# Optimization experiments

Hardware: AMD Instinct MI355X
Metric: run time of the kernel (lower is better)

## Reference

```python
import jax, jax.numpy as jnp
import numpy as np

CH = 256
IC = 128  # inter_channels = channels // reduction
TEMP = 0.05


def setup_inputs() -> dict:
    key = jax.random.key(0)
    k1, k2, k3, k4, k5 = jax.random.split(key, 5)
    x = jax.random.normal(k1, (8, CH, 64, 64), dtype=jnp.float32)
    # 1x1 conv weights stored as [out_ch, in_ch]
    w_qkv = jax.random.normal(k2, (3 * IC, CH), dtype=jnp.float32) * 0.01
    b_qkv = jax.random.normal(k3, (3 * IC,), dtype=jnp.float32) * 0.01
    w_out = jax.random.normal(k4, (CH, IC), dtype=jnp.float32) * 0.01
    b_out = jax.random.normal(k5, (CH,), dtype=jnp.float32) * 0.01
    return {"x": x, "w_qkv": w_qkv, "b_qkv": b_qkv, "w_out": w_out, "b_out": b_out}


def reference(x, w_qkv, b_qkv, w_out, b_out):
    b, c, h, w = x.shape
    n = h * w
    ic = w_qkv.shape[0] // 3
    # 1x1 conv QKV projection
    qkv = jnp.einsum('bchw,oc->bohw', x, w_qkv) + b_qkv[None, :, None, None]
    qkv = qkv.reshape(b, 3, ic, n)
    q, k, v = qkv[:, 0], qkv[:, 1], qkv[:, 2]  # each [b, ic, n]
    # mean-center q and k over spatial positions (per channel)
    k = k - k.mean(axis=-1, keepdims=True)
    q = q - q.mean(axis=-1, keepdims=True)
    # pairwise_weight[b, i, j] = sum_c k[b, c, i] * q[b, c, j]
    pw = jnp.einsum('bci,bcj->bij', k, q)
    pw = pw / jnp.sqrt(jnp.float32(ic))  # use_scale=True
    pw = pw / TEMP
    pw = jax.nn.softmax(pw, axis=-1)  # [b, n, n]
    # y[b, c, i] = sum_j pw[b, i, j] * v[b, c, j]
    y = jnp.einsum('bij,bcj->bci', pw, v).reshape(b, ic, h, w)
    out = x + jnp.einsum('bchw,oc->bohw', y, w_out) + b_out[None, :, None, None]
    return out
```

## Files before the change

### kernel.cpp

```cpp
#include <hip/hip_runtime.h>
#include <hip/hip_bf16.h>

typedef __bf16 bf16_t;
typedef __bf16 bf16x8 __attribute__((ext_vector_type(8)));
typedef float f32x4 __attribute__((ext_vector_type(4)));
typedef float f32x16 __attribute__((ext_vector_type(16)));

#define MFMA16(a, b, c) __builtin_amdgcn_mfma_f32_16x16x32_bf16((a), (b), (c), 0, 0, 0)
#define MFMA32(a, b, c) __builtin_amdgcn_mfma_f32_32x32x16_bf16((a), (b), (c), 0, 0, 0)

constexpr int BATCH = 8, CH = 256, IC = 128, NPOS = 4096;
constexpr float SM_C = 2.5503488f;

constexpr size_t OFF_XT    = 0;
constexpr size_t OFF_QT    = 16777216;
constexpr size_t OFF_KT    = 25165824;
constexpr size_t OFF_V     = 33554432;
constexpr size_t OFF_WQKV  = 41943040;
constexpr size_t OFF_WOUT  = 42139648;
constexpr size_t OFF_XMEAN = 42205184;
constexpr size_t OFF_QKM   = 42213376;
constexpr size_t OFF_PL    = 42221568;

__device__ __forceinline__ void gload_lds16(const char* g, char* lds) {
    __builtin_amdgcn_global_load_lds((const __attribute__((address_space(1))) unsigned int*)g,
                                     (__attribute__((address_space(3))) unsigned int*)lds, 16, 0,
                                     0);
}
__device__ __forceinline__ float fexp2(float x) {
    float r;
    asm("v_exp_f32 %0, %1" : "=v"(r) : "v"(x));
    return r;
}
__device__ __forceinline__ int cvtpk(float lo, float hi) {
    int r;
    asm("v_cvt_pk_bf16_f32 %0, %1, %2" : "=v"(r) : "v"(lo), "v"(hi));
    return r;
}

__global__ void k_convert_w(const float* __restrict__ wqkv, const float* __restrict__ wout,
                            bf16_t* __restrict__ wqkv_b, bf16_t* __restrict__ wout_b) {
    int idx = blockIdx.x * 256 + threadIdx.x;
    if (idx < 384 * 256) wqkv_b[idx] = (bf16_t)wqkv[idx];
    int j = idx - 384 * 256;
    if (j >= 0 && j < 256 * 128) wout_b[j] = (bf16_t)wout[j];
}

__global__ void k_xmean(const float* __restrict__ x, float* __restrict__ xmean) {
    int c = blockIdx.x, b = blockIdx.y;
    const float4* xv = (const float4*)(x + ((size_t)(b * CH + c)) * NPOS);
    float s = 0.f;
#pragma unroll
    for (int r = 0; r < 4; r++) {
        float4 v = xv[r * 256 + threadIdx.x];
        s += v.x + v.y + v.z + v.w;
    }
    __shared__ float red[256];
    red[threadIdx.x] = s;
    __syncthreads();
    for (int st = 128; st > 0; st >>= 1) {
        if (threadIdx.x < st) red[threadIdx.x] += red[threadIdx.x + st];
        __syncthreads();
    }
    if (threadIdx.x == 0) xmean[b * CH + c] = red[0] * (1.0f / NPOS);
}

__global__ void k_qkmean(const float* __restrict__ wqkv, const float* __restrict__ xmean,
                         float* __restrict__ qkm) {
    int o = blockIdx.x, b = blockIdx.y, lane = threadIdx.x;
    float4 w = ((const float4*)(wqkv + (size_t)o * CH))[lane];
    float4 xm = ((const float4*)(xmean + b * CH))[lane];
    float s = w.x * xm.x + w.y * xm.y + w.z * xm.z + w.w * xm.w;
#pragma unroll
    for (int m = 1; m < 64; m <<= 1) s += __shfl_xor(s, m, 64);
    if (lane == 0) qkm[b * CH + o] = s;
}

__global__ void k_transpose(const float* __restrict__ x, bf16_t* __restrict__ xt) {
    __shared__ float t[32][33];
    int p0 = blockIdx.x * 32, c0 = blockIdx.y * 32, b = blockIdx.z;
    int i = threadIdx.x >> 5, j = threadIdx.x & 31;
#pragma unroll
    for (int q = 0; q < 4; q++) {
        int c = c0 + q * 8 + i;
        t[q * 8 + i][j] = x[((size_t)(b * CH + c)) * NPOS + p0 + j];
    }
    __syncthreads();
#pragma unroll
    for (int q = 0; q < 4; q++) {
        int p = p0 + q * 8 + i;
        xt[((size_t)(b * NPOS + p)) * CH + c0 + j] = (bf16_t)t[j][q * 8 + i];
    }
}

__global__ __launch_bounds__(256, 2) void k_qkv(const bf16_t* __restrict__ xt,
                                                const bf16_t* __restrict__ wqkv_b,
                                                const float* __restrict__ qkm,
                                                const float* __restrict__ b_qkv,
                                                bf16_t* __restrict__ qt, bf16_t* __restrict__ kt,
                                                bf16_t* __restrict__ v) {
    int bid = blockIdx.x;
    int b = bid & 7;
    int r0 = bid >> 3;
    int sec = r0 % 3;
    int pt = r0 / 3;
    int p0 = pt * 128;
    int wid = threadIdx.x >> 6, lane = threadIdx.x & 63;
    int g = lane >> 4, li = lane & 15;
    int wr = wid >> 1, wc = wid & 1;
    f32x4 acc[4][4] = {};
    if (sec < 2) {
        int ob = sec * 128;
#pragma unroll 1
        for (int kk = 0; kk < 8; kk++) {
            bf16x8 af[4], bfg[4];
#pragma unroll
            for (int fa = 0; fa < 4; fa++) {
                int p = p0 + wr * 64 + fa * 16 + li;
                af[fa] = *(const bf16x8*)(xt + ((size_t)(b * NPOS + p)) * CH + kk * 32 + g * 8);
            }
#pragma unroll
            for (int fb = 0; fb < 4; fb++) {
                int o = ob + wc * 64 + fb * 16 + li;
                bfg[fb] = *(const bf16x8*)(wqkv_b + (size_t)o * CH + kk * 32 + g * 8);
            }
#pragma unroll
            for (int fa = 0; fa < 4; fa++)
#pragma unroll
                for (int fb = 0; fb < 4; fb++) acc[fa][fb] = MFMA16(af[fa], bfg[fb], acc[fa][fb]);
        }
        bf16_t* dst = (sec == 0) ? qt : kt;
        float scale = (sec == 1) ? SM_C : 1.0f;
#pragma unroll
        for (int fb = 0; fb < 4; fb++) {
            int ol = wc * 64 + fb * 16 + li;
            float mean = qkm[b * CH + sec * 128 + ol];
#pragma unroll
            for (int fa = 0; fa < 4; fa++)
#pragma unroll
                for (int r = 0; r < 4; r++) {
                    int p = p0 + wr * 64 + fa * 16 + g * 4 + r;
                    dst[((size_t)(b * NPOS + p)) * IC + ol] =
                        (bf16_t)((acc[fa][fb][r] - mean) * scale);
                }
        }
    } else {
#pragma unroll 1
        for (int kk = 0; kk < 8; kk++) {
            bf16x8 af[4], bfg[4];
#pragma unroll
            for (int fa = 0; fa < 4; fa++) {
                int o = 256 + wr * 64 + fa * 16 + li;
                af[fa] = *(const bf16x8*)(wqkv_b + (size_t)o * CH + kk * 32 + g * 8);
            }
#pragma unroll
            for (int fb = 0; fb < 4; fb++) {
                int p = p0 + wc * 64 + fb * 16 + li;
                bfg[fb] = *(const bf16x8*)(xt + ((size_t)(b * NPOS + p)) * CH + kk * 32 + g * 8);
            }
#pragma unroll
            for (int fa = 0; fa < 4; fa++)
#pragma unroll
                for (int fb = 0; fb < 4; fb++) acc[fa][fb] = MFMA16(af[fa], bfg[fb], acc[fa][fb]);
        }
#pragma unroll
        for (int fa = 0; fa < 4; fa++)
#pragma unroll
            for (int r = 0; r < 4; r++) {
                int oe = wr * 64 + fa * 16 + g * 4 + r;
                float bias = b_qkv[256 + oe];
#pragma unroll
                for (int fb = 0; fb < 4; fb++) {
                    int p = p0 + wc * 64 + fb * 16 + li;
                    v[((size_t)(b * IC + oe)) * NPOS + p] = (bf16_t)(acc[fa][fb][r] + bias);
                }
            }
    }
}

constexpr int TJ = 64;

__global__ __launch_bounds__(256, 2) void k_attn(const bf16_t* __restrict__ qt,
                                                 const bf16_t* __restrict__ kt,
                                                 const bf16_t* __restrict__ v,
                                                 bf16_t* __restrict__ pacc,
                                                 float* __restrict__ pl) {
    __shared__ __attribute__((aligned(128))) char smem[2 * 32768];
    const int bid = blockIdx.x;
    const int b = bid & 7;
    const int r0 = bid >> 3;
    const int jh = r0 & 1;
    const int it = r0 >> 1;
    const int jbase = jh * 2048;
    const int wid = threadIdx.x >> 6, lane = threadIdx.x & 63;
    const int col = lane & 31, h = lane >> 5;
    const int iw0 = it * 128 + wid * 32;
    const bf16_t* ktb = kt + (size_t)b * NPOS * IC;
    const bf16_t* qtb = qt + (size_t)b * NPOS * IC;
    const bf16_t* vb = v + (size_t)b * IC * NPOS;

    int qoff_[4], voff_[4];
#pragma unroll
    for (int u = 0; u < 4; u++) {
        int t = wid * 4 + u;
        int qrow = 4 * t + (lane >> 4);
        qoff_[u] = qrow * 256 + (((lane & 15) ^ (qrow & 7)) << 4);
        int vrow = 8 * t + (lane >> 3);
        voff_[u] = vrow * 8192 + (((lane & 7) ^ (vrow & 7)) << 4);
    }

    auto stage = [&](int dstpar, int sj) {
        const char* qs = (const char*)qtb + (size_t)sj * 256;
        const char* vs = (const char*)vb + (size_t)sj * 2;
        char* qd = smem + dstpar * 32768;
        char* vd = qd + 16384;
#pragma unroll
        for (int u = 0; u < 4; u++) {
            gload_lds16(qs + qoff_[u], qd + (wid * 4 + u) * 1024);
            gload_lds16(vs + voff_[u], vd + (wid * 4 + u) * 1024);
        }
    };

    stage(0, jbase);

    bf16x8 bk[8];
#pragma unroll
    for (int ks = 0; ks < 8; ks++)
        bk[ks] = *(const bf16x8*)(ktb + (size_t)(iw0 + col) * IC + ks * 16 + h * 8);

    f32x16 acc[4] = {};
    float ls[4] = {0.f, 0.f, 0.f, 0.f};

    auto body = [&](int par, int nextj) {
        stage(par ^ 1, nextj);
        asm volatile("s_waitcnt vmcnt(8)" ::: "memory");
        __builtin_amdgcn_s_barrier();
        asm volatile("" ::: "memory");
        const char* qb = smem + par * 32768;
        const char* vbuf = qb + 16384;
#pragma unroll
        for (int jsub = 0; jsub < 2; jsub++) {
            f32x16 s = {};
#pragma unroll
            for (int ks = 0; ks < 8; ks++) {
                bf16x8 aq = *(const bf16x8*)(qb + (jsub * 32 + col) * 256 +
                                             (((ks * 2 + h) ^ (col & 7)) << 4));
                s = MFMA32(aq, bk[ks], s);
            }
            float e[16];
#pragma unroll
            for (int r = 0; r < 16; r++) e[r] = fexp2(s[r]);
#pragma unroll
            for (int r = 0; r < 16; r++) ls[r & 3] += e[r];
            int w[8];
#pragma unroll
            for (int q = 0; q < 8; q++) w[q] = cvtpk(e[2 * q], e[2 * q + 1]);
            asm("v_permlane32_swap_b32 %0, %1" : "+v"(w[0]), "+v"(w[2]));
            asm("v_permlane32_swap_b32 %0, %1" : "+v"(w[1]), "+v"(w[3]));
            asm("v_permlane32_swap_b32 %0, %1" : "+v"(w[4]), "+v"(w[6]));
            asm("v_permlane32_swap_b32 %0, %1" : "+v"(w[5]), "+v"(w[7]));
            union {
                int u[4];
                bf16x8 v;
            } pb0, pb1;
            pb0.u[0] = w[0]; pb0.u[1] = w[1]; pb0.u[2] = w[2]; pb0.u[3] = w[3];
            pb1.u[0] = w[4]; pb1.u[1] = w[5]; pb1.u[2] = w[6]; pb1.u[3] = w[7];
#pragma unroll
            for (int kl = 0; kl < 2; kl++) {
                int kg = jsub * 2 + kl;
                bf16x8 pbf = kl == 0 ? pb0.v : pb1.v;
#pragma unroll
                for (int cs = 0; cs < 4; cs++) {
                    bf16x8 av = *(const bf16x8*)(vbuf + (cs * 32 + col) * 128 +
                                                 (((kg * 2 + h) ^ (col & 7)) << 4));
                    acc[cs] = MFMA32(av, pbf, acc[cs]);
                }
            }
        }
        asm volatile("" ::: "memory");
        __builtin_amdgcn_s_barrier();
    };

#pragma unroll 1
    for (int jo = 0; jo < 2048; jo += 2 * TJ) {
        body(0, jbase + ((jo + TJ) & 2047));
        body(1, jbase + ((jo + 2 * TJ) & 2047));
    }

    float lsum = (ls[0] + ls[1]) + (ls[2] + ls[3]);
    lsum += __shfl_xor(lsum, 32, 64);
    const int i = iw0 + col;
    if (h == 0) pl[((size_t)(b * 2 + jh)) * NPOS + i] = lsum;

    bf16_t* po = pacc + ((size_t)(b * 2 + jh)) * NPOS * IC;
#pragma unroll
    for (int cs = 0; cs < 4; cs++)
#pragma unroll
        for (int q = 0; q < 8; q++) {
            int u = cvtpk(acc[cs][2 * q], acc[cs][2 * q + 1]);
            int c0 = cs * 32 + ((q & 1) << 1) + ((q >> 1) << 3) + 4 * h;
            *(int*)((char*)po + ((size_t)i * IC + c0) * 2) = u;
        }
}

__global__ void k_merge(const bf16_t* __restrict__ pacc, const float* __restrict__ pl,
                        bf16_t* __restrict__ yt) {
    int idx = blockIdx.x * 256 + threadIdx.x;
    int co = idx & 15;
    int i = (idx >> 4) & 4095;
    int b = idx >> 16;
    const bf16x8* p0 = (const bf16x8*)pacc + ((size_t)(b * 2 + 0) * NPOS + i) * 16 + co;
    const bf16x8* p1 = (const bf16x8*)pacc + ((size_t)(b * 2 + 1) * NPOS + i) * 16 + co;
    float l = pl[(size_t)(b * 2 + 0) * NPOS + i] + pl[(size_t)(b * 2 + 1) * NPOS + i];
    float inv = 1.0f / l;
    bf16x8 a0 = *p0, a1 = *p1, o;
#pragma unroll
    for (int j = 0; j < 8; j++) o[j] = (bf16_t)(((float)a0[j] + (float)a1[j]) * inv);
    *((bf16x8*)yt + ((size_t)b * NPOS + i) * 16 + co) = o;
}

__global__ __launch_bounds__(256, 2) void k_out(const bf16_t* __restrict__ yt,
                                                const bf16_t* __restrict__ wout_b,
                                                const float* __restrict__ x,
                                                const float* __restrict__ b_out,
                                                float* __restrict__ out) {
    int bid = blockIdx.x;
    int b = bid & 7;
    int r0 = bid >> 3;
    int oct = r0 & 1, pt = r0 >> 1;
    int p0 = pt * 128, oc0 = oct * 128;
    int wid = threadIdx.x >> 6, lane = threadIdx.x & 63;
    int g = lane >> 4, li = lane & 15;
    int wr = wid >> 1, wc = wid & 1;
    f32x4 acc[4][4] = {};
#pragma unroll
    for (int kk = 0; kk < 4; kk++) {
        bf16x8 af[4], bfg[4];
#pragma unroll
        for (int fa = 0; fa < 4; fa++) {
            int oc = oc0 + wr * 64 + fa * 16 + li;
            af[fa] = *(const bf16x8*)(wout_b + (size_t)oc * IC + kk * 32 + g * 8);
        }
#pragma unroll
        for (int fb = 0; fb < 4; fb++) {
            int p = p0 + wc * 64 + fb * 16 + li;
            bfg[fb] = *(const bf16x8*)(yt + ((size_t)(b * NPOS + p)) * IC + kk * 32 + g * 8);
        }
#pragma unroll
        for (int fa = 0; fa < 4; fa++)
#pragma unroll
            for (int fb = 0; fb < 4; fb++) acc[fa][fb] = MFMA16(af[fa], bfg[fb], acc[fa][fb]);
    }
#pragma unroll
    for (int fa = 0; fa < 4; fa++)
#pragma unroll
        for (int r = 0; r < 4; r++) {
            int oc = oc0 + wr * 64 + fa * 16 + g * 4 + r;
            float bias = b_out[oc];
#pragma unroll
            for (int fb = 0; fb < 4; fb++) {
                int p = p0 + wc * 64 + fb * 16 + li;
                size_t idx = ((size_t)(b * CH + oc)) * NPOS + p;
                out[idx] = acc[fa][fb][r] + x[idx] + bias;
            }
        }
}

extern "C" void kernel_launch(void* const* d_in, const int* in_sizes, int n_in, void* d_out,
                              int out_size, void* d_ws, size_t ws_size, hipStream_t stream) {
    const float* x = (const float*)d_in[0];
    const float* w_qkv = (const float*)d_in[1];
    const float* b_qkv = (const float*)d_in[2];
    const float* w_out = (const float*)d_in[3];
    const float* b_out = (const float*)d_in[4];
    float* out = (float*)d_out;
    char* ws = (char*)d_ws;

    bf16_t* xt = (bf16_t*)(ws + OFF_XT);
    bf16_t* pacc = (bf16_t*)(ws + OFF_XT);
    bf16_t* qt = (bf16_t*)(ws + OFF_QT);
    bf16_t* kt = (bf16_t*)(ws + OFF_KT);
    bf16_t* yt = (bf16_t*)(ws + OFF_KT);
    bf16_t* v = (bf16_t*)(ws + OFF_V);
    bf16_t* wqkv_b = (bf16_t*)(ws + OFF_WQKV);
    bf16_t* wout_b = (bf16_t*)(ws + OFF_WOUT);
    float* xmean = (float*)(ws + OFF_XMEAN);
    float* qkm = (float*)(ws + OFF_QKM);
    float* pl = (float*)(ws + OFF_PL);

    k_convert_w<<<512, 256, 0, stream>>>(w_qkv, w_out, wqkv_b, wout_b);
    k_xmean<<<dim3(256, 8), 256, 0, stream>>>(x, xmean);
    k_qkmean<<<dim3(256, 8), 64, 0, stream>>>(w_qkv, xmean, qkm);
    k_transpose<<<dim3(128, 8, 8), 256, 0, stream>>>(x, xt);
    k_qkv<<<768, 256, 0, stream>>>(xt, wqkv_b, qkm, b_qkv, qt, kt, v);
    k_attn<<<512, 256, 0, stream>>>(qt, kt, v, pacc, pl);
    k_merge<<<2048, 256, 0, stream>>>(pacc, pl, yt);
    k_out<<<512, 256, 0, stream>>>(yt, wout_b, x, b_out, out);
}
```

Before: 149.2 us.

## Split attention waves over j with 2x i-tiles and fuse merge into output projection

Each attention wave now handles 64 query rows and half of the 64-column j tile instead of 32 rows and the full tile. Each Q and V fragment read from LDS therefore feeds two MFMAs, which halves LDS reads per MFMA. The two j-halves are reduced through shared memory at the end, and s_setprio hints are added around the MFMA phases. The separate k_merge kernel is removed: k_out now sums the two partial accumulators and normalizes them on load, saving a launch and a round trip through global memory. The cost is doubled register use for the K fragments and accumulators, which puts the 2-blocks-per-CU occupancy at risk, plus an extra LDS reduction epilogue.

```diff
diff --git a/kernel.cpp b/kernel.cpp
--- a/kernel.cpp
+++ b/kernel.cpp
@@ -185,7 +185,7 @@
                                                  const bf16_t* __restrict__ v,
                                                  bf16_t* __restrict__ pacc,
                                                  float* __restrict__ pl) {
-    __shared__ __attribute__((aligned(128))) char smem[2 * 32768];
+    __shared__ __attribute__((aligned(128))) char smem[2 * 32768 + 4096];
     const int bid = blockIdx.x;
     const int b = bid & 7;
     const int r0 = bid >> 3;
@@ -194,7 +194,8 @@
     const int jbase = jh * 2048;
     const int wid = threadIdx.x >> 6, lane = threadIdx.x & 63;
     const int col = lane & 31, h = lane >> 5;
-    const int iw0 = it * 128 + wid * 32;
+    const int jw = wid >> 1, ih = wid & 1;
+    const int iwW = it * 128 + ih * 64;
     const bf16_t* ktb = kt + (size_t)b * NPOS * IC;
     const bf16_t* qtb = qt + (size_t)b * NPOS * IC;
     const bf16_t* vb = v + (size_t)b * IC * NPOS;
@@ -223,13 +224,38 @@
 
     stage(0, jbase);
 
-    bf16x8 bk[8];
-#pragma unroll
-    for (int ks = 0; ks < 8; ks++)
-        bk[ks] = *(const bf16x8*)(ktb + (size_t)(iw0 + col) * IC + ks * 16 + h * 8);
-
-    f32x16 acc[4] = {};
-    float ls[4] = {0.f, 0.f, 0.f, 0.f};
+    bf16x8 bk0[8], bk1[8];
+#pragma unroll
+    for (int ks = 0; ks < 8; ks++) {
+        bk0[ks] = *(const bf16x8*)(ktb + (size_t)(iwW + col) * IC + ks * 16 + h * 8);
+        bk1[ks] = *(const bf16x8*)(ktb + (size_t)(iwW + 32 + col) * IC + ks * 16 + h * 8);
+    }
+
+    f32x16 acc0[4] = {}, acc1[4] = {};
+    float ls0[4] = {}, ls1[4] = {};
+
+    auto packP = [&](const f32x16& s, float* lsx, bf16x8& o0, bf16x8& o1) {
+        float e[16];
+#pragma unroll
+        for (int r = 0; r < 16; r++) e[r] = fexp2(s[r]);
+#pragma unroll
+        for (int r = 0; r < 16; r++) lsx[r & 3] += e[r];
+        int w[8];
+#pragma unroll
+        for (int q = 0; q < 8; q++) w[q] = cvtpk(e[2 * q], e[2 * q + 1]);
+        asm("v_permlane32_swap_b32 %0, %1" : "+v"(w[0]), "+v"(w[2]));
+        asm("v_permlane32_swap_b32 %0, %1" : "+v"(w[1]), "+v"(w[3]));
+        asm("v_permlane32_swap_b32 %0, %1" : "+v"(w[4]), "+v"(w[6]));
+        asm("v_permlane32_swap_b32 %0, %1" : "+v"(w[5]), "+v"(w[7]));
+        union {
+            int u[4];
+            bf16x8 v;
+        } t0, t1;
+        t0.u[0] = w[0]; t0.u[1] = w[1]; t0.u[2] = w[2]; t0.u[3] = w[3];
+        t1.u[0] = w[4]; t1.u[1] = w[5]; t1.u[2] = w[6]; t1.u[3] = w[7];
+        o0 = t0.v;
+        o1 = t1.v;
+    };
 
     auto body = [&](int par, int nextj) {
         stage(par ^ 1, nextj);
@@ -238,45 +264,34 @@
         asm volatile("" ::: "memory");
         const char* qb = smem + par * 32768;
         const char* vbuf = qb + 16384;
-#pragma unroll
-        for (int jsub = 0; jsub < 2; jsub++) {
-            f32x16 s = {};
-#pragma unroll
-            for (int ks = 0; ks < 8; ks++) {
-                bf16x8 aq = *(const bf16x8*)(qb + (jsub * 32 + col) * 256 +
-                                             (((ks * 2 + h) ^ (col & 7)) << 4));
-                s = MFMA32(aq, bk[ks], s);
-            }
-            float e[16];
-#pragma unroll
-            for (int r = 0; r < 16; r++) e[r] = fexp2(s[r]);
-#pragma unroll
-            for (int r = 0; r < 16; r++) ls[r & 3] += e[r];
-            int w[8];
-#pragma unroll
-            for (int q = 0; q < 8; q++) w[q] = cvtpk(e[2 * q], e[2 * q + 1]);
-            asm("v_permlane32_swap_b32 %0, %1" : "+v"(w[0]), "+v"(w[2]));
-            asm("v_permlane32_swap_b32 %0, %1" : "+v"(w[1]), "+v"(w[3]));
-            asm("v_permlane32_swap_b32 %0, %1" : "+v"(w[4]), "+v"(w[6]));
-            asm("v_permlane32_swap_b32 %0, %1" : "+v"(w[5]), "+v"(w[7]));
-            union {
-                int u[4];
-                bf16x8 v;
-            } pb0, pb1;
-            pb0.u[0] = w[0]; pb0.u[1] = w[1]; pb0.u[2] = w[2]; pb0.u[3] = w[3];
-            pb1.u[0] = w[4]; pb1.u[1] = w[5]; pb1.u[2] = w[6]; pb1.u[3] = w[7];
-#pragma unroll
-            for (int kl = 0; kl < 2; kl++) {
-                int kg = jsub * 2 + kl;
-                bf16x8 pbf = kl == 0 ? pb0.v : pb1.v;
-#pragma unroll
-                for (int cs = 0; cs < 4; cs++) {
-                    bf16x8 av = *(const bf16x8*)(vbuf + (cs * 32 + col) * 128 +
-                                                 (((kg * 2 + h) ^ (col & 7)) << 4));
-                    acc[cs] = MFMA32(av, pbf, acc[cs]);
-                }
-            }
-        }
+        f32x16 sA = {}, sB = {};
+        __builtin_amdgcn_s_setprio(1);
+#pragma unroll
+        for (int ks = 0; ks < 8; ks++) {
+            bf16x8 aq = *(const bf16x8*)(qb + (jw * 32 + col) * 256 +
+                                         (((ks * 2 + h) ^ (col & 7)) << 4));
+            sA = MFMA32(aq, bk0[ks], sA);
+            sB = MFMA32(aq, bk1[ks], sB);
+        }
+        __builtin_amdgcn_s_setprio(0);
+        bf16x8 pA0, pA1, pB0, pB1;
+        packP(sA, ls0, pA0, pA1);
+        packP(sB, ls1, pB0, pB1);
+        __builtin_amdgcn_s_setprio(1);
+#pragma unroll
+        for (int kl = 0; kl < 2; kl++) {
+            int kg = jw * 2 + kl;
+            bf16x8 pA = kl ? pA1 : pA0;
+            bf16x8 pB = kl ? pB1 : pB0;
+#pragma unroll
+            for (int cs = 0; cs < 4; cs++) {
+                bf16x8 av = *(const bf16x8*)(vbuf + (cs * 32 + col) * 128 +
+                                             (((kg * 2 + h) ^ (col & 7)) << 4));
+                acc0[cs] = MFMA32(av, pA, acc0[cs]);
+                acc1[cs] = MFMA32(av, pB, acc1[cs]);
+            }
+        }
+        __builtin_amdgcn_s_setprio(0);
         asm volatile("" ::: "memory");
         __builtin_amdgcn_s_barrier();
     };
@@ -287,39 +302,62 @@
         body(1, jbase + ((jo + 2 * TJ) & 2047));
     }
 
-    float lsum = (ls[0] + ls[1]) + (ls[2] + ls[3]);
-    lsum += __shfl_xor(lsum, 32, 64);
-    const int i = iw0 + col;
-    if (h == 0) pl[((size_t)(b * 2 + jh)) * NPOS + i] = lsum;
-
-    bf16_t* po = pacc + ((size_t)(b * 2 + jh)) * NPOS * IC;
-#pragma unroll
-    for (int cs = 0; cs < 4; cs++)
-#pragma unroll
-        for (int q = 0; q < 8; q++) {
-            int u = cvtpk(acc[cs][2 * q], acc[cs][2 * q + 1]);
-            int c0 = cs * 32 + ((q & 1) << 1) + ((q >> 1) << 3) + 4 * h;
-            *(int*)((char*)po + ((size_t)i * IC + c0) * 2) = u;
-        }
-}
-
-__global__ void k_merge(const bf16_t* __restrict__ pacc, const float* __restrict__ pl,
-                        bf16_t* __restrict__ yt) {
-    int idx = blockIdx.x * 256 + threadIdx.x;
-    int co = idx & 15;
-    int i = (idx >> 4) & 4095;
-    int b = idx >> 16;
-    const bf16x8* p0 = (const bf16x8*)pacc + ((size_t)(b * 2 + 0) * NPOS + i) * 16 + co;
-    const bf16x8* p1 = (const bf16x8*)pacc + ((size_t)(b * 2 + 1) * NPOS + i) * 16 + co;
-    float l = pl[(size_t)(b * 2 + 0) * NPOS + i] + pl[(size_t)(b * 2 + 1) * NPOS + i];
-    float inv = 1.0f / l;
-    bf16x8 a0 = *p0, a1 = *p1, o;
-#pragma unroll
-    for (int j = 0; j < 8; j++) o[j] = (bf16_t)(((float)a0[j] + (float)a1[j]) * inv);
-    *((bf16x8*)yt + ((size_t)b * NPOS + i) * 16 + co) = o;
-}
-
-__global__ __launch_bounds__(256, 2) void k_out(const bf16_t* __restrict__ yt,
+    asm volatile("s_waitcnt vmcnt(0)" ::: "memory");
+    __syncthreads();
+    float* lb = (float*)(smem + 65536);
+    if (jw == 1) {
+        float* db = (float*)(smem + ih * 32768);
+#pragma unroll
+        for (int it2 = 0; it2 < 2; it2++)
+#pragma unroll
+            for (int cs = 0; cs < 4; cs++) {
+                const f32x16 A = it2 ? acc1[cs] : acc0[cs];
+#pragma unroll
+                for (int q = 0; q < 4; q++) {
+                    f32x4 tv = {A[4 * q], A[4 * q + 1], A[4 * q + 2], A[4 * q + 3]};
+                    *(f32x4*)(db + ((it2 * 4 + cs) * 4 + q) * 256 + lane * 4) = tv;
+                }
+            }
+        lb[(ih * 2 + 0) * 64 + lane] = (ls0[0] + ls0[1]) + (ls0[2] + ls0[3]);
+        lb[(ih * 2 + 1) * 64 + lane] = (ls1[0] + ls1[1]) + (ls1[2] + ls1[3]);
+    }
+    __syncthreads();
+    if (jw == 0) {
+        const float* db = (const float*)(smem + ih * 32768);
+        float lsA = (ls0[0] + ls0[1]) + (ls0[2] + ls0[3]) + lb[(ih * 2 + 0) * 64 + lane];
+        float lsB = (ls1[0] + ls1[1]) + (ls1[2] + ls1[3]) + lb[(ih * 2 + 1) * 64 + lane];
+        lsA += __shfl_xor(lsA, 32, 64);
+        lsB += __shfl_xor(lsB, 32, 64);
+        if (h == 0) {
+            pl[((size_t)(b * 2 + jh)) * NPOS + iwW + col] = lsA;
+            pl[((size_t)(b * 2 + jh)) * NPOS + iwW + 32 + col] = lsB;
+        }
+        bf16_t* po = pacc + ((size_t)(b * 2 + jh)) * NPOS * IC;
+#pragma unroll
+        for (int it2 = 0; it2 < 2; it2++) {
+            int i = iwW + it2 * 32 + col;
+#pragma unroll
+            for (int cs = 0; cs < 4; cs++) {
+                f32x16 A = it2 ? acc1[cs] : acc0[cs];
+#pragma unroll
+                for (int q = 0; q < 4; q++) {
+                    f32x4 r = *(const f32x4*)(db + ((it2 * 4 + cs) * 4 + q) * 256 + lane * 4);
+#pragma unroll
+                    for (int e = 0; e < 4; e++) A[4 * q + e] += r[e];
+                }
+#pragma unroll
+                for (int q = 0; q < 8; q++) {
+                    int u = cvtpk(A[2 * q], A[2 * q + 1]);
+                    int c0 = cs * 32 + ((q & 1) << 1) + ((q >> 1) << 3) + 4 * h;
+                    *(int*)((char*)po + ((size_t)i * IC + c0) * 2) = u;
+                }
+            }
+        }
+    }
+}
+
+__global__ __launch_bounds__(256, 2) void k_out(const bf16_t* __restrict__ pacc,
+                                                const float* __restrict__ pl,
                                                 const bf16_t* __restrict__ wout_b,
                                                 const float* __restrict__ x,
                                                 const float* __restrict__ b_out,
@@ -332,6 +370,14 @@
     int wid = threadIdx.x >> 6, lane = threadIdx.x & 63;
     int g = lane >> 4, li = lane & 15;
     int wr = wid >> 1, wc = wid & 1;
+    const bf16_t* pa0 = pacc + (size_t)(b * 2 + 0) * NPOS * IC;
+    const bf16_t* pa1 = pacc + (size_t)(b * 2 + 1) * NPOS * IC;
+    float inv[4];
+#pragma unroll
+    for (int fb = 0; fb < 4; fb++) {
+        int p = p0 + wc * 64 + fb * 16 + li;
+        inv[fb] = 1.0f / (pl[(size_t)(b * 2 + 0) * NPOS + p] + pl[(size_t)(b * 2 + 1) * NPOS + p]);
+    }
     f32x4 acc[4][4] = {};
 #pragma unroll
     for (int kk = 0; kk < 4; kk++) {
@@ -344,7 +390,11 @@
 #pragma unroll
         for (int fb = 0; fb < 4; fb++) {
             int p = p0 + wc * 64 + fb * 16 + li;
-            bfg[fb] = *(const bf16x8*)(yt + ((size_t)(b * NPOS + p)) * IC + kk * 32 + g * 8);
+            bf16x8 a0 = *(const bf16x8*)(pa0 + (size_t)p * IC + kk * 32 + g * 8);
+            bf16x8 a1 = *(const bf16x8*)(pa1 + (size_t)p * IC + kk * 32 + g * 8);
+#pragma unroll
+            for (int e = 0; e < 8; e++)
+                bfg[fb][e] = (bf16_t)(((float)a0[e] + (float)a1[e]) * inv[fb]);
         }
 #pragma unroll
         for (int fa = 0; fa < 4; fa++)
@@ -380,7 +430,6 @@
     bf16_t* pacc = (bf16_t*)(ws + OFF_XT);
     bf16_t* qt = (bf16_t*)(ws + OFF_QT);
     bf16_t* kt = (bf16_t*)(ws + OFF_KT);
-    bf16_t* yt = (bf16_t*)(ws + OFF_KT);
     bf16_t* v = (bf16_t*)(ws + OFF_V);
     bf16_t* wqkv_b = (bf16_t*)(ws + OFF_WQKV);
     bf16_t* wout_b = (bf16_t*)(ws + OFF_WOUT);
@@ -394,6 +443,5 @@
     k_transpose<<<dim3(128, 8, 8), 256, 0, stream>>>(x, xt);
     k_qkv<<<768, 256, 0, stream>>>(xt, wqkv_b, qkm, b_qkv, qt, kt, v);
     k_attn<<<512, 256, 0, stream>>>(qt, kt, v, pacc, pl);
-    k_merge<<<2048, 256, 0, stream>>>(pacc, pl, yt);
-    k_out<<<512, 256, 0, stream>>>(yt, wout_b, x, b_out, out);
-}
+    k_out<<<512, 256, 0, stream>>>(pacc, pl, wout_b, x, b_out, out);
+}
```

New measurement: 258.3 us. 73.1% more time.
